# Performance work log

Measured on AMD Instinct MI355X. Metric: run time of the kernel, lower is better.

The kernel has to match this reference:

```python
import jax, jax.numpy as jnp
import numpy as np

HEAD, D_MODEL, D_KV = 16, 1024, 64
B, NQ, NK = 2, 2048, 2048


def setup_inputs() -> dict:
    key = jax.random.key(0)
    ks = jax.random.split(key, 10)
    s = 1.0 / np.sqrt(D_MODEL)
    return {
        "queries": jax.random.normal(ks[0], (B, NQ, D_MODEL), jnp.float32),
        "keys": jax.random.normal(ks[1], (B, NK, D_MODEL), jnp.float32),
        "values": jax.random.normal(ks[2], (B, NK, D_MODEL), jnp.float32),
        "group_prob": jax.random.uniform(ks[3], (B, 1, NQ, NK), jnp.float32),
        "attention_mask": jnp.ones((B, NK), jnp.int32),
        "Wq": jax.random.normal(ks[4], (D_MODEL, HEAD * D_KV), jnp.float32) * s,
        "bq": jnp.zeros((HEAD * D_KV,), jnp.float32),
        "Wk": jax.random.normal(ks[5], (D_MODEL, HEAD * D_KV), jnp.float32) * s,
        "bk": jnp.zeros((HEAD * D_KV,), jnp.float32),
        "Wv": jax.random.normal(ks[6], (D_MODEL, HEAD * D_KV), jnp.float32) * s,
        "bv": jnp.zeros((HEAD * D_KV,), jnp.float32),
    }


def reference(queries, keys, values, group_prob, attention_mask, Wq, bq, Wk, bk, Wv, bv):
    b_s, nq, _ = queries.shape
    nk = keys.shape[1]
    # projections -> [b, h, n, d]
    q = (queries @ Wq + bq).reshape(b_s, nq, HEAD, D_KV).transpose(0, 2, 1, 3)
    k = (keys @ Wk + bk).reshape(b_s, nk, HEAD, D_KV).transpose(0, 2, 1, 3)
    v = (values @ Wv + bv).reshape(b_s, nk, HEAD, D_KV).transpose(0, 2, 1, 3)
    att = jnp.einsum("bhqd,bhkd->bhqk", q, k) / np.sqrt(D_KV).astype(np.float32)
    # NOTE: original uses non-in-place `att.masked_fill(...)` and discards the
    # result, so attention_mask has NO effect on the computation. Replicated.
    att = jax.nn.softmax(att, axis=-1)
    att = att * group_prob  # post-softmax group gating, broadcast over heads
    out = jnp.einsum("bhqk,bhkd->bhqd", att, v)
    return out.transpose(0, 2, 1, 3).reshape(b_s, nq, D_MODEL)
```

## Files before the change

kernel.cpp:

```cpp
#include <hip/hip_runtime.h>
#include <hip/hip_bf16.h>
#include <cstdint>

typedef unsigned short ushort_t;
typedef __attribute__((ext_vector_type(8))) short short8;
typedef __attribute__((ext_vector_type(4))) float floatx4;
typedef __attribute__((ext_vector_type(4))) unsigned short ushort4_t;

#define H_   16
#define DKV_ 64
#define DM_  1024
#define B_   2
#define NQ_  2048
#define NK_  2048

__device__ __forceinline__ unsigned short f2bf(float f) {
  union { float f; unsigned int u; } v; v.f = f;
  unsigned int u = v.u;
  return (unsigned short)((u + 0x7fffu + ((u >> 16) & 1u)) >> 16);
}

__device__ __forceinline__ float fexp2(float x) { return __builtin_amdgcn_exp2f(x); }
__device__ __forceinline__ float frcp(float x)  { return __builtin_amdgcn_rcpf(x); }

__device__ __forceinline__ floatx4 mfma16(short8 a, short8 b, floatx4 c) {
  return __builtin_amdgcn_mfma_f32_16x16x32_bf16(a, b, c, 0, 0, 0);
}

__device__ __forceinline__ void gload_lds16(const ushort_t* g, ushort_t* l) {
  __builtin_amdgcn_global_load_lds(
      (const __attribute__((address_space(1))) void*)g,
      (__attribute__((address_space(3))) void*)l, 16, 0, 0);
}

__device__ __forceinline__ void block_sync_lds() {
  asm volatile("s_waitcnt lgkmcnt(0)" ::: "memory");
  __builtin_amdgcn_s_barrier();
  __builtin_amdgcn_sched_barrier(0);
}

__global__ __launch_bounds__(256) void cast_x_kernel(
    const float* __restrict__ q, const float* __restrict__ k,
    const float* __restrict__ v, ushort_t* __restrict__ dst)
{
  const int t = blockIdx.y;
  const float* src = (t == 0) ? q : (t == 1) ? k : v;
  ushort_t* d = dst + (size_t)t * 4096 * 1024;
  const int gid = blockIdx.x * 256 + threadIdx.x;
  #pragma unroll
  for (int u = 0; u < 8; u++) {
    const int i4 = u * 131072 + gid;
    floatx4 f = ((const floatx4*)src)[i4];
    ushort4_t o;
    #pragma unroll
    for (int e = 0; e < 4; e++) o[e] = f2bf(f[e]);
    *(ushort4_t*)&d[(size_t)i4 * 4] = o;
  }
}

__global__ __launch_bounds__(256) void cast_wt_kernel(
    const float* __restrict__ Wq, const float* __restrict__ Wk,
    const float* __restrict__ Wv, ushort_t* __restrict__ WtAll)
{
  __shared__ ushort_t tile[32][33];
  const int t = blockIdx.z;
  const float* W = (t == 0) ? Wq : (t == 1) ? Wk : Wv;
  ushort_t* Wt = WtAll + (size_t)t * 1024 * 1024;
  const int n0 = blockIdx.x * 32, k0 = blockIdx.y * 32;
  const int tid = threadIdx.x, r = tid >> 3, c4 = (tid & 7) * 4;
  floatx4 f = *(const floatx4*)&W[(size_t)(k0 + r) * 1024 + n0 + c4];
  #pragma unroll
  for (int e = 0; e < 4; e++) tile[r][c4 + e] = f2bf(f[e]);
  __syncthreads();
  ushort4_t o;
  #pragma unroll
  for (int e = 0; e < 4; e++) o[e] = tile[c4 + e][r];
  *(ushort4_t*)&Wt[(size_t)(n0 + r) * 1024 + k0 + c4] = o;
}

__global__ __launch_bounds__(256, 2) void proj_kernel2(
    const ushort_t* __restrict__ Xbf, const ushort_t* __restrict__ WtAll,
    const float* __restrict__ bq, const float* __restrict__ bk,
    const float* __restrict__ bv,
    ushort_t* __restrict__ Qb, ushort_t* __restrict__ Kb, ushort_t* __restrict__ Vt)
{
  const int mode = blockIdx.z;
  const ushort_t* X  = Xbf  + (size_t)mode * 4096 * 1024;
  const ushort_t* Wt = WtAll + (size_t)mode * 1024 * 1024;
  const float* bias  = (mode == 0) ? bq : (mode == 1) ? bk : bv;
  ushort_t* dst      = (mode == 0) ? Qb : (mode == 1) ? Kb : Vt;

  __shared__ ushort_t SM[16384];

  const int tid = threadIdx.x, lane = tid & 63, wid = tid >> 6;
  const int c = lane & 15, g = lane >> 4;
  const int m0 = blockIdx.y * 128, n0 = blockIdx.x * 128;
  const int wm = wid & 1, wn = wid >> 1, mb = wm * 64, nb = wn * 64;
  const int srow = lane >> 2;
  const int schunk = (lane & 3) * 8;

  floatx4 acc[4][4];
  #pragma unroll
  for (int i = 0; i < 4; i++)
    #pragma unroll
    for (int j = 0; j < 4; j++) acc[i][j] = floatx4{0.f, 0.f, 0.f, 0.f};

  #pragma unroll
  for (int u = 0; u < 2; u++) {
    const int t = wid * 2 + u;
    gload_lds16(&X [(size_t)(m0 + t * 16 + srow) * 1024 + schunk], &SM[t * 512]);
    gload_lds16(&Wt[(size_t)(n0 + t * 16 + srow) * 1024 + schunk], &SM[4096 + t * 512]);
  }
  __syncthreads();

  for (int step = 0; step < 32; step++) {
    const int cur = step & 1, nxt = cur ^ 1;
    if (step + 1 < 32) {
      const int k1 = (step + 1) * 32;
      #pragma unroll
      for (int u = 0; u < 2; u++) {
        const int t = wid * 2 + u;
        gload_lds16(&X [(size_t)(m0 + t * 16 + srow) * 1024 + k1 + schunk],
                    &SM[nxt * 8192 + t * 512]);
        gload_lds16(&Wt[(size_t)(n0 + t * 16 + srow) * 1024 + k1 + schunk],
                    &SM[nxt * 8192 + 4096 + t * 512]);
      }
    }
    const ushort_t* SA = &SM[cur * 8192];
    const ushort_t* SB = &SM[cur * 8192 + 4096];
    short8 af[4], bfr[4];
    #pragma unroll
    for (int i = 0; i < 4; i++) af[i]  = *(const short8*)&SA[(mb + i * 16 + c) * 32 + g * 8];
    #pragma unroll
    for (int j = 0; j < 4; j++) bfr[j] = *(const short8*)&SB[(nb + j * 16 + c) * 32 + g * 8];
    #pragma unroll
    for (int i = 0; i < 4; i++)
      #pragma unroll
      for (int j = 0; j < 4; j++) acc[i][j] = mfma16(af[i], bfr[j], acc[i][j]);
    __syncthreads();
  }

  const float scale = (mode == 0) ? 0.18033688011112042f : 1.0f;
  ushort_t* EP = SM + wid * 2048;
  const int hh = (n0 + nb) >> 6;

  if (mode != 2) {
    for (int jj = 0; jj < 2; jj++) {
      #pragma unroll
      for (int jt = 0; jt < 2; jt++) {
        const int j = jj * 2 + jt;
        const float bb = bias[n0 + nb + j * 16 + c];
        #pragma unroll
        for (int i = 0; i < 4; i++)
          #pragma unroll
          for (int r = 0; r < 4; r++)
            EP[(i * 16 + g * 4 + r) * 32 + jt * 16 + c] =
                f2bf((acc[i][j][r] + bb) * scale);
      }
      #pragma unroll
      for (int u = 0; u < 8; u++) {
        const int rowl = u * 8 + (lane >> 3);
        ushort4_t vv = *(ushort4_t*)&EP[rowl * 32 + (lane & 7) * 4];
        const int rowg = m0 + mb + rowl;
        const int bb2 = rowg >> 11, nn = rowg & 2047;
        *(ushort4_t*)&dst[((size_t)(bb2 * H_ + hh) * NQ_ + nn) * DKV_ +
                          jj * 32 + (lane & 7) * 4] = vv;
      }
    }
  } else {
    const int bb2 = (m0 + mb) >> 11, nloc = (m0 + mb) & 2047;
    for (int j = 0; j < 4; j++) {
      const float bb = bias[n0 + nb + j * 16 + c];
      #pragma unroll
      for (int i = 0; i < 4; i++) {
        ushort4_t pk;
        #pragma unroll
        for (int r = 0; r < 4; r++) pk[r] = f2bf(acc[i][j][r] + bb);
        *(ushort4_t*)&EP[c * 72 + i * 16 + g * 4] = pk;
      }
      const int d0 = j * 16;
      #pragma unroll
      for (int u = 0; u < 2; u++) {
        const int coll = u * 8 + (lane >> 3);
        short8 vv = *(const short8*)&EP[coll * 72 + (lane & 7) * 8];
        *(short8*)&dst[((size_t)(bb2 * H_ + hh) * DKV_ + d0 + coll) * NK_ +
                       nloc + (lane & 7) * 8] = vv;
      }
    }
  }
}

constexpr int LDT = 40;
__global__ __launch_bounds__(256, 2) void proj_kernel_fb(
    const float* __restrict__ Xq, const float* __restrict__ Xk, const float* __restrict__ Xv,
    const float* __restrict__ Wq, const float* __restrict__ Wk, const float* __restrict__ Wv,
    const float* __restrict__ bq, const float* __restrict__ bk, const float* __restrict__ bv,
    ushort_t* __restrict__ Qb, ushort_t* __restrict__ Kb, ushort_t* __restrict__ Vt)
{
  const int mode = blockIdx.z;
  const float* X    = (mode == 0) ? Xq : (mode == 1) ? Xk : Xv;
  const float* W    = (mode == 0) ? Wq : (mode == 1) ? Wk : Wv;
  const float* bias = (mode == 0) ? bq : (mode == 1) ? bk : bv;
  ushort_t* dst     = (mode == 0) ? Qb : (mode == 1) ? Kb : Vt;

  __shared__ ushort_t Asm[128 * LDT];
  __shared__ ushort_t Bsm[128 * LDT];

  const int tid = threadIdx.x, lane = tid & 63, wid = tid >> 6;
  const int m0 = blockIdx.y * 128, n0 = blockIdx.x * 128;
  const int c = lane & 15, g = lane >> 4;
  const int wm = wid & 1, wn = wid >> 1, mb = wm * 64, nb = wn * 64;

  floatx4 acc[4][4];
  #pragma unroll
  for (int i = 0; i < 4; i++)
    #pragma unroll
    for (int j = 0; j < 4; j++) acc[i][j] = floatx4{0.f, 0.f, 0.f, 0.f};

  const int ar = tid >> 1, ah = tid & 1;
  const int bn = tid & 127, bh2 = tid >> 7;

  for (int k0 = 0; k0 < DM_; k0 += 32) {
    const floatx4* ap = (const floatx4*)(X + (size_t)(m0 + ar) * DM_ + k0 + ah * 16);
    floatx4 av0 = ap[0], av1 = ap[1], av2 = ap[2], av3 = ap[3];
    const float* wp = W + (size_t)(k0 + bh2 * 16) * 1024 + n0 + bn;
    float wv[16];
    #pragma unroll
    for (int j = 0; j < 16; j++) wv[j] = wp[j * 1024];
    short8 pa0, pa1, pb0, pb1;
    #pragma unroll
    for (int j = 0; j < 4; j++) {
      pa0[j] = (short)f2bf(av0[j]); pa0[4 + j] = (short)f2bf(av1[j]);
      pa1[j] = (short)f2bf(av2[j]); pa1[4 + j] = (short)f2bf(av3[j]);
    }
    #pragma unroll
    for (int j = 0; j < 8; j++) { pb0[j] = (short)f2bf(wv[j]); pb1[j] = (short)f2bf(wv[8 + j]); }
    __syncthreads();
    *(short8*)&Asm[ar * LDT + ah * 16]      = pa0;
    *(short8*)&Asm[ar * LDT + ah * 16 + 8]  = pa1;
    *(short8*)&Bsm[bn * LDT + bh2 * 16]     = pb0;
    *(short8*)&Bsm[bn * LDT + bh2 * 16 + 8] = pb1;
    __syncthreads();
    short8 af[4], bfr[4];
    #pragma unroll
    for (int i = 0; i < 4; i++) af[i]  = *(const short8*)&Asm[(mb + i * 16 + c) * LDT + g * 8];
    #pragma unroll
    for (int j = 0; j < 4; j++) bfr[j] = *(const short8*)&Bsm[(nb + j * 16 + c) * LDT + g * 8];
    #pragma unroll
    for (int i = 0; i < 4; i++)
      #pragma unroll
      for (int j = 0; j < 4; j++) acc[i][j] = mfma16(af[i], bfr[j], acc[i][j]);
  }
  #pragma unroll
  for (int j = 0; j < 4; j++) {
    const int col = n0 + nb + j * 16 + c;
    const float bv_ = bias[col];
    const int h = col >> 6, d = col & 63;
    #pragma unroll
    for (int i = 0; i < 4; i++)
      #pragma unroll
      for (int r = 0; r < 4; r++) {
        const int row = m0 + mb + i * 16 + g * 4 + r;
        const int b = row >> 11, n = row & 2047;
        float v = acc[i][j][r] + bv_;
        if (mode == 0) {
          v *= 0.18033688011112042f;
          dst[((size_t)(b * H_ + h) * NQ_ + n) * DKV_ + d] = f2bf(v);
        } else if (mode == 1) {
          dst[((size_t)(b * H_ + h) * NQ_ + n) * DKV_ + d] = f2bf(v);
        } else {
          dst[((size_t)(b * H_ + h) * DKV_ + d) * NK_ + n] = f2bf(v);
        }
      }
  }
}

__global__ __launch_bounds__(512, 4) void attn_kernel(
    const ushort_t* __restrict__ Qb, const ushort_t* __restrict__ Kb,
    const ushort_t* __restrict__ Vt, const float* __restrict__ gp,
    float* __restrict__ out)
{
  __shared__ ushort_t Ks[2][64 * 72];
  __shared__ ushort_t Vs[2][64 * 72];
  __shared__ ushort_t Pl[8][16 * 72];

  constexpr int NT = NK_ / 64;

  const int tid = threadIdx.x, lane = tid & 63, wid = tid >> 6;
  const int c = lane & 15, g = lane >> 4;
  const int h = blockIdx.x, b = blockIdx.z;
  const int bh = b * H_ + h;
  const int qw = blockIdx.y * 128 + wid * 16;

  const ushort_t* Qp = Qb + (size_t)bh * NQ_ * DKV_;
  const ushort_t* Kp = Kb + (size_t)bh * NK_ * DKV_;
  const ushort_t* Vp = Vt + (size_t)bh * DKV_ * NK_;
  const float* gpp = gp + (size_t)b * NQ_ * NK_ + (size_t)qw * NK_;
  ushort_t* Pw = Pl[wid];

  const int gx16 = (g >> 1) << 4;
  const int prd  = g ^ (((c >> 3) & 1) << 1);

  const int srow = tid >> 3;
  const int scol = (tid & 7) * 8;

  short8 qf[2];
  #pragma unroll
  for (int kc = 0; kc < 2; kc++)
    qf[kc] = *(const short8*)&Qp[(qw + c) * DKV_ + kc * 32 + g * 8];

  *(short8*)&Ks[0][srow * 72 + scol] = *(const short8*)&Kp[(size_t)srow * DKV_ + scol];
  *(short8*)&Vs[0][srow * 72 + scol] = *(const short8*)&Vp[(size_t)srow * NK_ + scol];
  float gpA[4][4], gpB[4][4];
  #pragma unroll
  for (int r = 0; r < 4; r++) {
    const float* gq = gpp + (size_t)(g * 4 + r) * NK_ + c;
    #pragma unroll
    for (int jk = 0; jk < 4; jk++) gpA[jk][r] = gq[jk * 16];
  }
  __syncthreads();

  floatx4 o[4];
  float l[4];
  #pragma unroll
  for (int jd = 0; jd < 4; jd++) o[jd] = floatx4{0.f, 0.f, 0.f, 0.f};
  #pragma unroll
  for (int r = 0; r < 4; r++) l[r] = 0.f;

#define ATTN_BODY(T, CUR, GPC, GPN)                                          \
  {                                                                          \
    const int t_ = (T);                                                      \
    const int k0 = t_ * 64;                                                  \
    const bool hn = (t_ + 1) < NT;                                           \
                        \
    short8 knx, vnx;                                                         \
    if (hn) {                                                                \
      const int k1 = k0 + 64;                                                \
      knx = *(const short8*)&Kp[(size_t)(k1 + srow) * DKV_ + scol];          \
      vnx = *(const short8*)&Vp[(size_t)srow * NK_ + k1 + scol];             \
    }                                                                        \
       \
    if (hn) {                                                                \
      const int k1 = k0 + 64;                                                \
      _Pragma("unroll")                                                      \
      for (int r = 0; r < 4; r++) {                                          \
        const float* gq = gpp + (size_t)(g * 4 + r) * NK_ + k1 + c;          \
        _Pragma("unroll")                                                    \
        for (int jk = 0; jk < 4; jk++) GPN[jk][r] = gq[jk * 16];             \
      }                                                                      \
    }                                                                        \
                                    \
    floatx4 s_[4];                                                           \
    _Pragma("unroll")                                                        \
    for (int jk = 0; jk < 4; jk++) s_[jk] = floatx4{0.f, 0.f, 0.f, 0.f};     \
    _Pragma("unroll")                                                        \
    for (int jk = 0; jk < 4; jk++)                                           \
      _Pragma("unroll")                                                      \
      for (int kc = 0; kc < 2; kc++) {                                       \
        short8 kf = *(const short8*)&Ks[CUR][(jk * 16 + c) * 72 + kc * 32 + g * 8]; \
        s_[jk] = mfma16(qf[kc], kf, s_[jk]);                                 \
      }                                                                      \
              \
    _Pragma("unroll")                                                        \
    for (int jk = 0; jk < 4; jk++) {                                         \
      const int colw = (jk << 4) ^ gx16;                                     \
      _Pragma("unroll")                                                      \
      for (int r = 0; r < 4; r++) {                                          \
        const float p = fexp2(s_[jk][r]);                                    \
        l[r] += p;                                                           \
        Pw[(g * 4 + r) * 72 + colw + c] = f2bf(p * GPC[jk][r]);              \
      }                                                                      \
    }                                                                        \
                         \
    _Pragma("unroll")                                                        \
    for (int kc = 0; kc < 2; kc++) {                                         \
      short8 af = *(const short8*)&Pw[c * 72 + kc * 32 + prd * 8];           \
      _Pragma("unroll")                                                      \
      for (int jd = 0; jd < 4; jd++) {                                       \
        short8 vf = *(const short8*)&Vs[CUR][(jd * 16 + c) * 72 + kc * 32 + g * 8]; \
        o[jd] = mfma16(af, vf, o[jd]);                                       \
      }                                                                      \
    }                                                                        \
     \
    if (hn) {                                                                \
      *(short8*)&Ks[(CUR) ^ 1][srow * 72 + scol] = knx;                      \
      *(short8*)&Vs[(CUR) ^ 1][srow * 72 + scol] = vnx;                      \
    }                                                                        \
    block_sync_lds();                                                        \
  }

  for (int tt = 0; tt < NT; tt += 2) {
    ATTN_BODY(tt,     0, gpA, gpB)
    ATTN_BODY(tt + 1, 1, gpB, gpA)
  }
#undef ATTN_BODY

  float invl[4];
  #pragma unroll
  for (int r = 0; r < 4; r++) {
    float rs = l[r];
    rs += __shfl_xor(rs, 1);
    rs += __shfl_xor(rs, 2);
    rs += __shfl_xor(rs, 4);
    rs += __shfl_xor(rs, 8);
    invl[r] = frcp(rs);
  }
  #pragma unroll
  for (int jd = 0; jd < 4; jd++)
    #pragma unroll
    for (int r = 0; r < 4; r++) {
      const int row = qw + g * 4 + r;
      out[(size_t)(b * NQ_ + row) * 1024 + h * 64 + jd * 16 + c] =
          o[jd][r] * invl[r];
    }
}

extern "C" void kernel_launch(void* const* d_in, const int* in_sizes, int n_in,
                              void* d_out, int out_size, void* d_ws, size_t ws_size,
                              hipStream_t stream) {
  const float* queries = (const float*)d_in[0];
  const float* keys    = (const float*)d_in[1];
  const float* values  = (const float*)d_in[2];
  const float* gp      = (const float*)d_in[3];
  const float* Wq = (const float*)d_in[5];
  const float* bq = (const float*)d_in[6];
  const float* Wk = (const float*)d_in[7];
  const float* bk = (const float*)d_in[8];
  const float* Wv = (const float*)d_in[9];
  const float* bv = (const float*)d_in[10];

  const size_t SZ_QKV = (size_t)3 * B_ * H_ * NQ_ * DKV_;
  const size_t SZ_X   = (size_t)3 * 4096 * 1024;
  const size_t SZ_W   = (size_t)3 * 1024 * 1024;
  const size_t NEED   = (SZ_QKV + SZ_X + SZ_W) * sizeof(ushort_t);

  ushort_t* Qb = (ushort_t*)d_ws;
  ushort_t* Kb = Qb + (size_t)B_ * H_ * NQ_ * DKV_;
  ushort_t* Vt = Kb + (size_t)B_ * H_ * NK_ * DKV_;
  float* out = (float*)d_out;

  if (ws_size >= NEED) {
    ushort_t* Xbf = Qb + SZ_QKV;
    ushort_t* Wt  = Xbf + SZ_X;
    cast_x_kernel<<<dim3(512, 3), 256, 0, stream>>>(queries, keys, values, Xbf);
    cast_wt_kernel<<<dim3(32, 32, 3), 256, 0, stream>>>(Wq, Wk, Wv, Wt);
    proj_kernel2<<<dim3(8, 32, 3), 256, 0, stream>>>(
        Xbf, Wt, bq, bk, bv, Qb, Kb, Vt);
  } else {
    proj_kernel_fb<<<dim3(8, 32, 3), 256, 0, stream>>>(
        queries, keys, values, Wq, Wk, Wv, bq, bk, bv, Qb, Kb, Vt);
  }
  attn_kernel<<<dim3(H_, NQ_ / 128, B_), 512, 0, stream>>>(Qb, Kb, Vt, gp, out);
}
```

Before: 244.4 us.

## Merge cast kernels into one launch and raise wave priority around MFMA blocks

Combines the activation-cast and weight-transpose-cast kernels into a single prep kernel that dispatches on block index, removing one kernel launch and its tail. In the attention loop, s_setprio raises wave priority around the QK and PV MFMA sections so matrix work is issued ahead of the exp/softmax work of other waves. The merged kernel puts the shared-memory tile allocation on every block, including the pure cast blocks, and the priority hints may not change scheduling much.

```diff
diff --git a/kernel.cpp b/kernel.cpp
--- a/kernel.cpp
+++ b/kernel.cpp
@@ -39,43 +39,46 @@
   __builtin_amdgcn_sched_barrier(0);
 }
 
-__global__ __launch_bounds__(256) void cast_x_kernel(
+__global__ __launch_bounds__(256) void prep_kernel(
     const float* __restrict__ q, const float* __restrict__ k,
-    const float* __restrict__ v, ushort_t* __restrict__ dst)
-{
-  const int t = blockIdx.y;
-  const float* src = (t == 0) ? q : (t == 1) ? k : v;
-  ushort_t* d = dst + (size_t)t * 4096 * 1024;
-  const int gid = blockIdx.x * 256 + threadIdx.x;
-  #pragma unroll
-  for (int u = 0; u < 8; u++) {
-    const int i4 = u * 131072 + gid;
-    floatx4 f = ((const floatx4*)src)[i4];
-    ushort4_t o;
-    #pragma unroll
-    for (int e = 0; e < 4; e++) o[e] = f2bf(f[e]);
-    *(ushort4_t*)&d[(size_t)i4 * 4] = o;
-  }
-}
-
-__global__ __launch_bounds__(256) void cast_wt_kernel(
+    const float* __restrict__ v,
     const float* __restrict__ Wq, const float* __restrict__ Wk,
-    const float* __restrict__ Wv, ushort_t* __restrict__ WtAll)
+    const float* __restrict__ Wv,
+    ushort_t* __restrict__ Xdst, ushort_t* __restrict__ WtAll)
 {
   __shared__ ushort_t tile[32][33];
-  const int t = blockIdx.z;
-  const float* W = (t == 0) ? Wq : (t == 1) ? Wk : Wv;
-  ushort_t* Wt = WtAll + (size_t)t * 1024 * 1024;
-  const int n0 = blockIdx.x * 32, k0 = blockIdx.y * 32;
-  const int tid = threadIdx.x, r = tid >> 3, c4 = (tid & 7) * 4;
-  floatx4 f = *(const floatx4*)&W[(size_t)(k0 + r) * 1024 + n0 + c4];
-  #pragma unroll
-  for (int e = 0; e < 4; e++) tile[r][c4 + e] = f2bf(f[e]);
-  __syncthreads();
-  ushort4_t o;
-  #pragma unroll
-  for (int e = 0; e < 4; e++) o[e] = tile[c4 + e][r];
-  *(ushort4_t*)&Wt[(size_t)(n0 + r) * 1024 + k0 + c4] = o;
+  const int bid = blockIdx.x;
+  if (bid < 1536) {
+    const int t = bid >> 9;
+    const float* src = (t == 0) ? q : (t == 1) ? k : v;
+    ushort_t* d = Xdst + (size_t)t * 4096 * 1024;
+    const int gid = (bid & 511) * 256 + threadIdx.x;
+    #pragma unroll
+    for (int u = 0; u < 8; u++) {
+      const int i4 = u * 131072 + gid;
+      floatx4 f = ((const floatx4*)src)[i4];
+      ushort4_t o;
+      #pragma unroll
+      for (int e = 0; e < 4; e++) o[e] = f2bf(f[e]);
+      *(ushort4_t*)&d[(size_t)i4 * 4] = o;
+    }
+  } else {
+    const int b2 = bid - 1536;
+    const int t = b2 >> 10;
+    const int rem = b2 & 1023;
+    const float* W = (t == 0) ? Wq : (t == 1) ? Wk : Wv;
+    ushort_t* Wt = WtAll + (size_t)t * 1024 * 1024;
+    const int n0 = (rem & 31) * 32, k0 = (rem >> 5) * 32;
+    const int tid = threadIdx.x, r = tid >> 3, c4 = (tid & 7) * 4;
+    floatx4 f = *(const floatx4*)&W[(size_t)(k0 + r) * 1024 + n0 + c4];
+    #pragma unroll
+    for (int e = 0; e < 4; e++) tile[r][c4 + e] = f2bf(f[e]);
+    __syncthreads();
+    ushort4_t o;
+    #pragma unroll
+    for (int e = 0; e < 4; e++) o[e] = tile[c4 + e][r];
+    *(ushort4_t*)&Wt[(size_t)(n0 + r) * 1024 + k0 + c4] = o;
+  }
 }
 
 __global__ __launch_bounds__(256, 2) void proj_kernel2(
@@ -353,6 +356,7 @@
     floatx4 s_[4];                                                           \
     _Pragma("unroll")                                                        \
     for (int jk = 0; jk < 4; jk++) s_[jk] = floatx4{0.f, 0.f, 0.f, 0.f};     \
+    __builtin_amdgcn_s_setprio(1);                                           \
     _Pragma("unroll")                                                        \
     for (int jk = 0; jk < 4; jk++)                                           \
       _Pragma("unroll")                                                      \
@@ -360,6 +364,7 @@
         short8 kf = *(const short8*)&Ks[CUR][(jk * 16 + c) * 72 + kc * 32 + g * 8]; \
         s_[jk] = mfma16(qf[kc], kf, s_[jk]);                                 \
       }                                                                      \
+    __builtin_amdgcn_s_setprio(0);                                           \
               \
     _Pragma("unroll")                                                        \
     for (int jk = 0; jk < 4; jk++) {                                         \
@@ -372,6 +377,7 @@
       }                                                                      \
     }                                                                        \
                          \
+    __builtin_amdgcn_s_setprio(1);                                           \
     _Pragma("unroll")                                                        \
     for (int kc = 0; kc < 2; kc++) {                                         \
       short8 af = *(const short8*)&Pw[c * 72 + kc * 32 + prd * 8];           \
@@ -381,6 +387,7 @@
         o[jd] = mfma16(af, vf, o[jd]);                                       \
       }                                                                      \
     }                                                                        \
+    __builtin_amdgcn_s_setprio(0);                                           \
      \
     if (hn) {                                                                \
       *(short8*)&Ks[(CUR) ^ 1][srow * 72 + scol] = knx;                      \
@@ -442,8 +449,8 @@
   if (ws_size >= NEED) {
     ushort_t* Xbf = Qb + SZ_QKV;
     ushort_t* Wt  = Xbf + SZ_X;
-    cast_x_kernel<<<dim3(512, 3), 256, 0, stream>>>(queries, keys, values, Xbf);
-    cast_wt_kernel<<<dim3(32, 32, 3), 256, 0, stream>>>(Wq, Wk, Wv, Wt);
+    prep_kernel<<<dim3(4608), 256, 0, stream>>>(
+        queries, keys, values, Wq, Wk, Wv, Xbf, Wt);
     proj_kernel2<<<dim3(8, 32, 3), 256, 0, stream>>>(
         Xbf, Wt, bq, bk, bv, Qb, Kb, Vt);
   } else {
```

Measured after the change: 240.9 us. About the same (-1.4%).
